# Kernel tuning notes

Hardware: AMD Instinct MI355X
Metric: run time of the kernel (lower is better)

Reference implementation:

```python
import jax, jax.numpy as jnp
import numpy as np

B, C_IN, S = 32, 4, 2048
NF = 256          # CNN filters
H = 256           # LSTM hidden per direction
NH, DH = 8, 64    # heads, single-head size
MH = 512          # multihead size
KSZ, PAD, POOL = 13, 6, 6
SP = (S + 2 * PAD - KSZ + 1) // POOL  # 341: post conv(len-preserving)+maxpool1d length


def _lstm_dir(x, Wih, Whh, b):
    # x: [T, N, C] -- torch LSTM gate order i,f,g,o; b = b_ih + b_hh merged
    N = x.shape[1]
    h0 = jnp.zeros((N, H), x.dtype)
    c0 = jnp.zeros((N, H), x.dtype)

    def step(carry, xt):
        h, c = carry
        g = xt @ Wih.T + h @ Whh.T + b
        i, f, gg, o = jnp.split(g, 4, axis=-1)
        c = jax.nn.sigmoid(f) * c + jax.nn.sigmoid(i) * jnp.tanh(gg)
        h = jax.nn.sigmoid(o) * jnp.tanh(c)
        return (h, c), h

    _, hs = jax.lax.scan(step, (h0, c0), x)
    return hs


def _bilstm(x, Wih, Whh, b):
    fwd = _lstm_dir(x, Wih[0], Whh[0], b[0])
    bwd = _lstm_dir(x[::-1], Wih[1], Whh[1], b[1])[::-1]
    return jnp.concatenate([fwd, bwd], axis=-1)


def _rpe():
    # RelativePosition: |clip(k-q, -(S-1), S-1)| / (S-1); identical across the
    # batch-repeat channels, so compute once then broadcast (same math).
    r = jnp.arange(S)
    d = jnp.abs(jnp.clip(r[None, :] - r[:, None], -(S - 1), S - 1))
    d = d.astype(jnp.float32) / jnp.float32(S - 1)
    # nn.MaxPool2d((9,9), stride=(6,6), padding=1) -> [341, 341]
    return jax.lax.reduce_window(d, -jnp.inf, jax.lax.max, (9, 9), (6, 6), [(1, 1), (1, 1)])


def setup_inputs():
    key = jax.random.key(0)
    ks = jax.random.split(key, 20)
    f = lambda i, shape: jax.random.normal(ks[i], shape, jnp.float32) * 0.05
    return {
        "inputs": jax.random.normal(ks[0], (B, C_IN, S), jnp.float32),
        "conv1_w": f(1, (NF, C_IN, KSZ)),
        "bn1_gamma": jnp.ones((NF,), jnp.float32),
        "bn1_beta": jnp.zeros((NF,), jnp.float32),
        "Wih0": f(2, (2, 4 * H, NF)),
        "Whh0": f(3, (2, 4 * H, H)),
        "b0": f(4, (2, 4 * H)),
        "Wih1": f(5, (2, 4 * H, 2 * H)),
        "Whh1": f(6, (2, 4 * H, H)),
        "b1": f(7, (2, 4 * H)),
        "Qw": f(8, (NH, DH, 2 * H)), "Qb": f(9, (NH, DH)),
        "Kw": f(10, (NH, DH, 2 * H)), "Kb": f(11, (NH, DH)),
        "Vw": f(12, (NH, DH, 2 * H)), "Vb": f(13, (NH, DH)),
        "mh_w": f(14, (MH, NH * DH)), "mh_b": f(15, (MH,)),
    }


def reference(inputs, conv1_w, bn1_gamma, bn1_beta, Wih0, Whh0, b0,
              Wih1, Whh1, b1, Qw, Qb, Kw, Kb, Vw, Vb, mh_w, mh_b):
    # layer1: Conv1d (bias=False, pad=6 keeps length) + BatchNorm1d(eval: mean=0, var=1) + ReLU + MaxPool1d(6)
    x = jax.lax.conv_general_dilated(inputs, conv1_w, (1,), [(PAD, PAD)],
                                     dimension_numbers=('NCH', 'OIH', 'NCH'))
    x = x * (bn1_gamma / jnp.sqrt(1.0 + 1e-5))[None, :, None] + bn1_beta[None, :, None]
    x = jax.nn.relu(x)
    x = jax.lax.reduce_window(x, -jnp.inf, jax.lax.max, (1, 1, POOL), (1, 1, POOL), 'VALID')  # [B,NF,SP]
    x = jnp.transpose(x, (0, 2, 1))  # [B, SP, NF]

    # torch nn.LSTM with batch_first=False fed [B,SP,NF]: scans over axis 0 (batch) -- replicated faithfully.
    x = _bilstm(x, Wih0, Whh0, b0)
    x = _bilstm(x, Wih1, Whh1, b1)  # [B, SP, 2H]
    # (the F_RNN/R_RNN split-and-concat is an identity)

    # per-head Q/K/V (batched over heads), relative attention, dropout off (eval)
    q = jnp.einsum('bsc,hdc->hbsd', x, Qw) + Qb[:, None, None, :]
    k = jnp.einsum('bsc,hdc->hbsd', x, Kw) + Kb[:, None, None, :]
    v = jnp.einsum('bsc,hdc->hbsd', x, Vw) + Vb[:, None, None, :]
    scores = jnp.einsum('hbqd,hbkd->hbqk', q, k) / jnp.sqrt(jnp.float32(DH))
    scores = scores / _rpe()[None, None, :, :]
    p = jax.nn.softmax(scores, axis=-1)
    attn = jax.nn.relu(jnp.einsum('hbqk,hbkd->hbqd', p, v))  # [NH,B,SP,DH]
    cat = jnp.transpose(attn, (1, 2, 0, 3)).reshape(B, SP, NH * DH)
    out = jax.nn.relu(cat @ mh_w.T + mh_b)  # MultiHeadLinear + MHReLU
    return out
```

## Files before the change

kernel.cpp:

```cpp
#include <hip/hip_runtime.h>
#include <math.h>

#define B_    32
#define CIN   4
#define SLEN  2048
#define NF    256
#define HD    256
#define SP    341
#define RTOT  (B_*SP)
#define NH_   8
#define DH_   64
#define GRP   4
#define PSTR  344
#define HS    (SP*HD)

typedef __attribute__((ext_vector_type(8))) short short8;
typedef __attribute__((ext_vector_type(4))) float floatx4;
typedef __attribute__((ext_vector_type(4))) unsigned short ushortx4;

__device__ __forceinline__ float sigmoidf_(float x) { return 1.0f / (1.0f + expf(-x)); }

__device__ __forceinline__ unsigned short f2bf(float x) {
    unsigned int u = __float_as_uint(x);
    unsigned int r = (u + 0x7FFF + ((u >> 16) & 1)) >> 16;
    return (unsigned short)r;
}
__device__ __forceinline__ float bf2f(unsigned short b) {
    return __uint_as_float(((unsigned int)b) << 16);
}

__global__ __launch_bounds__(256)
void conv_pool_k(const float* __restrict__ in, const float* __restrict__ cw,
                 const float* __restrict__ gamma, const float* __restrict__ beta,
                 float* __restrict__ x0)
{
    const int b  = blockIdx.y;
    const int s0 = blockIdx.x * 16;
    const int co = threadIdx.x;
    __shared__ float ins[CIN][16*6 + 12];
    for (int idx = threadIdx.x; idx < CIN*108; idx += 256) {
        int ci = idx / 108, o = idx % 108;
        int pos = 6*s0 - 6 + o;
        ins[ci][o] = (pos >= 0 && pos < SLEN) ? in[(b*CIN + ci)*SLEN + pos] : 0.0f;
    }
    float wreg[52];
    {
        const float4* wp = (const float4*)(cw + co*52);
        #pragma unroll
        for (int j4 = 0; j4 < 13; ++j4) {
            float4 w4 = wp[j4];
            wreg[j4*4+0]=w4.x; wreg[j4*4+1]=w4.y; wreg[j4*4+2]=w4.z; wreg[j4*4+3]=w4.w;
        }
    }
    const float scale = gamma[co] * (1.0f / sqrtf(1.0f + 1e-5f));
    const float shift = beta[co];
    __syncthreads();
    for (int si = 0; si < 16; ++si) {
        int s = s0 + si;
        if (s >= SP) break;
        float win[CIN][18];
        #pragma unroll
        for (int ci = 0; ci < CIN; ++ci)
            #pragma unroll
            for (int o = 0; o < 18; ++o)
                win[ci][o] = ins[ci][6*si + o];
        float m = -1e30f;
        #pragma unroll
        for (int p6 = 0; p6 < 6; ++p6) {
            float acc = 0.0f;
            #pragma unroll
            for (int ci = 0; ci < CIN; ++ci)
                #pragma unroll
                for (int kk = 0; kk < 13; ++kk)
                    acc += win[ci][p6+kk] * wreg[ci*13+kk];
            float val = acc * scale + shift;
            val = fmaxf(val, 0.0f);
            m = fmaxf(m, val);
        }
        x0[(size_t)(b*SP + s)*NF + co] = m;
    }
}

__global__ __launch_bounds__(256)
void pack4_k(const float* __restrict__ W, unsigned short* __restrict__ hi,
             unsigned short* __restrict__ lo, int n4)
{
    int i = blockIdx.x * 256 + threadIdx.x;
    if (i >= n4) return;
    float4 x = *((const float4*)W + i);
    float v[4] = {x.x, x.y, x.z, x.w};
    ushortx4 h, l;
    #pragma unroll
    for (int e = 0; e < 4; ++e) {
        unsigned short hb = f2bf(v[e]);
        h[e] = hb;
        l[e] = f2bf(v[e] - bf2f(hb));
    }
    *((ushortx4*)hi + i) = h;
    *((ushortx4*)lo + i) = l;
}

template<int RELU>
__global__ __launch_bounds__(256)
void gemm_bf_k(const unsigned short* __restrict__ Ahi, const unsigned short* __restrict__ Alo,
               const unsigned short* __restrict__ Bhi, const unsigned short* __restrict__ Blo,
               const float* __restrict__ bias, float* __restrict__ C,
               int M, int N, int K)
{
    const int n0 = blockIdx.x * 128;
    const int m0 = blockIdx.y * 128;
    const int tid = threadIdx.x;
    const int lane = tid & 63;
    const int w = tid >> 6;
    const int wm = w >> 1, wn = w & 1;
    const int ln15 = lane & 15, lq = lane >> 4;

    __shared__ unsigned short AsH[128][40];
    __shared__ unsigned short AsL[128][40];
    __shared__ unsigned short BsH[128][40];
    __shared__ unsigned short BsL[128][40];

    floatx4 acc[4][4];
    #pragma unroll
    for (int i = 0; i < 4; ++i)
        #pragma unroll
        for (int j = 0; j < 4; ++j) acc[i][j] = (floatx4){0.f, 0.f, 0.f, 0.f};

    const int srow = tid >> 2;
    const int scol = (tid & 3) * 8;
    int ra0 = m0 + srow;      if (ra0 >= M) ra0 = M - 1;
    int ra1 = m0 + srow + 64; if (ra1 >= M) ra1 = M - 1;
    const int rb0 = n0 + srow;
    const int rb1 = n0 + srow + 64;

    for (int k0 = 0; k0 < K; k0 += 32) {
        const size_t aoff0 = (size_t)ra0*K + k0 + scol;
        const size_t aoff1 = (size_t)ra1*K + k0 + scol;
        const size_t boff0 = (size_t)rb0*K + k0 + scol;
        const size_t boff1 = (size_t)rb1*K + k0 + scol;
        short8 ah0 = *(const short8*)(Ahi + aoff0);
        short8 ah1 = *(const short8*)(Ahi + aoff1);
        short8 al0 = *(const short8*)(Alo + aoff0);
        short8 al1 = *(const short8*)(Alo + aoff1);
        short8 bh0 = *(const short8*)(Bhi + boff0);
        short8 bh1 = *(const short8*)(Bhi + boff1);
        short8 bl0 = *(const short8*)(Blo + boff0);
        short8 bl1 = *(const short8*)(Blo + boff1);
        *(short8*)&AsH[srow     ][scol] = ah0;
        *(short8*)&AsH[srow + 64][scol] = ah1;
        *(short8*)&AsL[srow     ][scol] = al0;
        *(short8*)&AsL[srow + 64][scol] = al1;
        *(short8*)&BsH[srow     ][scol] = bh0;
        *(short8*)&BsH[srow + 64][scol] = bh1;
        *(short8*)&BsL[srow     ][scol] = bl0;
        *(short8*)&BsL[srow + 64][scol] = bl1;
        __syncthreads();

        short8 fa_h[4], fa_l[4], fb_h[4], fb_l[4];
        #pragma unroll
        for (int mt = 0; mt < 4; ++mt) {
            fa_h[mt] = *(const short8*)&AsH[wm*64 + mt*16 + ln15][lq*8];
            fa_l[mt] = *(const short8*)&AsL[wm*64 + mt*16 + ln15][lq*8];
        }
        #pragma unroll
        for (int nt = 0; nt < 4; ++nt) {
            fb_h[nt] = *(const short8*)&BsH[wn*64 + nt*16 + ln15][lq*8];
            fb_l[nt] = *(const short8*)&BsL[wn*64 + nt*16 + ln15][lq*8];
        }
        #pragma unroll
        for (int mt = 0; mt < 4; ++mt)
            #pragma unroll
            for (int nt = 0; nt < 4; ++nt) {
                acc[mt][nt] = __builtin_amdgcn_mfma_f32_16x16x32_bf16(fa_l[mt], fb_h[nt], acc[mt][nt], 0, 0, 0);
                acc[mt][nt] = __builtin_amdgcn_mfma_f32_16x16x32_bf16(fa_h[mt], fb_l[nt], acc[mt][nt], 0, 0, 0);
                acc[mt][nt] = __builtin_amdgcn_mfma_f32_16x16x32_bf16(fa_h[mt], fb_h[nt], acc[mt][nt], 0, 0, 0);
            }
        __syncthreads();
    }

    #pragma unroll
    for (int nt = 0; nt < 4; ++nt) {
        const int n = n0 + wn*64 + nt*16 + ln15;
        const float bv = bias[n];
        #pragma unroll
        for (int mt = 0; mt < 4; ++mt) {
            const int mbase = m0 + wm*64 + mt*16 + lq*4;
            #pragma unroll
            for (int r = 0; r < 4; ++r) {
                int m = mbase + r;
                if (m < M) {
                    float val = acc[mt][nt][r] + bv;
                    if (RELU) val = fmaxf(val, 0.0f);
                    C[(size_t)m*N + n] = val;
                }
            }
        }
    }
}

__global__ __launch_bounds__(256)
void lstm_step_mfma_k(const float* __restrict__ G,
                      const unsigned short* __restrict__ Whi,
                      const unsigned short* __restrict__ Wlo,
                      const float* __restrict__ h_in,
                      float* __restrict__ h_out,
                      float* __restrict__ c_st,
                      float* __restrict__ x_out,
                      int s)
{
    const int j0 = blockIdx.x * 32;
    const int m0 = blockIdx.y * 32;
    const int d  = blockIdx.z;
    const int t_in = d ? (B_ - 1 - s) : s;
    const int tid = threadIdx.x;
    const int w = tid >> 6, lane = tid & 63;
    const int mhalf = w & 1, gpair = w >> 1;
    const int ln15 = lane & 15, lq = lane >> 4;

    __shared__ float Csh[32][132];

    int am = m0 + mhalf*16 + ln15; if (am > SP-1) am = SP-1;
    const int akoff = lq * 8;
    const float* hA = h_in + (size_t)d*HS + (size_t)am*HD;

    const unsigned short* WhiD = Whi + (size_t)d*1024*256;
    const unsigned short* WloD = Wlo + (size_t)d*1024*256;
    int nrow[4];
    #pragma unroll
    for (int t = 0; t < 4; ++t)
        nrow[t] = (gpair*2 + (t>>1))*256 + j0 + (t&1)*16 + ln15;

    floatx4 acc[4];
    #pragma unroll
    for (int t = 0; t < 4; ++t) acc[t] = (floatx4){0.f, 0.f, 0.f, 0.f};

    #pragma unroll
    for (int kk = 0; kk < 8; ++kk) {
        const int ko = kk*32 + akoff;
        float4 v0 = *(const float4*)(hA + ko);
        float4 v1 = *(const float4*)(hA + ko + 4);
        float vv[8] = {v0.x, v0.y, v0.z, v0.w, v1.x, v1.y, v1.z, v1.w};
        short8 ahi, alo;
        #pragma unroll
        for (int e = 0; e < 8; ++e) {
            unsigned short hb16 = f2bf(vv[e]);
            ahi[e] = (short)hb16;
            alo[e] = (short)f2bf(vv[e] - bf2f(hb16));
        }
        #pragma unroll
        for (int t = 0; t < 4; ++t) {
            short8 bhi = *(const short8*)(WhiD + (size_t)nrow[t]*HD + ko);
            short8 blo = *(const short8*)(WloD + (size_t)nrow[t]*HD + ko);
            acc[t] = __builtin_amdgcn_mfma_f32_16x16x32_bf16(alo, bhi, acc[t], 0, 0, 0);
            acc[t] = __builtin_amdgcn_mfma_f32_16x16x32_bf16(ahi, blo, acc[t], 0, 0, 0);
            acc[t] = __builtin_amdgcn_mfma_f32_16x16x32_bf16(ahi, bhi, acc[t], 0, 0, 0);
        }
    }

    #pragma unroll
    for (int t = 0; t < 4; ++t) {
        int col = gpair*64 + (t>>1)*32 + (t&1)*16 + ln15;
        int rb  = mhalf*16 + lq*4;
        #pragma unroll
        for (int r = 0; r < 4; ++r)
            Csh[rb + r][col] = acc[t][r];
    }
    __syncthreads();

    const int emloc = tid >> 3;
    const int ej4   = (tid & 7) * 4;
    const int em    = m0 + emloc;
    if (em < SP) {
        size_t gb = ((size_t)t_in*SP + em)*2048 + (size_t)d*1024 + j0 + ej4;
        float4 gi4 = *(const float4*)&G[gb];
        float4 gf4 = *(const float4*)&G[gb + 256];
        float4 gg4 = *(const float4*)&G[gb + 512];
        float4 go4 = *(const float4*)&G[gb + 768];
        size_t cbase = ((size_t)d*SP + em)*HD + j0 + ej4;
        float4 cold = *(float4*)&c_st[cbase];
        float hv[4];
        #pragma unroll
        for (int e = 0; e < 4; ++e) {
            float gi = Csh[emloc][     ej4+e] + (&gi4.x)[e];
            float gf = Csh[emloc][32 + ej4+e] + (&gf4.x)[e];
            float gg = Csh[emloc][64 + ej4+e] + (&gg4.x)[e];
            float go = Csh[emloc][96 + ej4+e] + (&go4.x)[e];
            float cn = sigmoidf_(gf)*(&cold.x)[e] + sigmoidf_(gi)*tanhf(gg);
            (&cold.x)[e] = cn;
            hv[e] = sigmoidf_(go)*tanhf(cn);
        }
        *(float4*)&c_st[cbase] = cold;
        float4 ho; ho.x = hv[0]; ho.y = hv[1]; ho.z = hv[2]; ho.w = hv[3];
        *(float4*)&h_out[cbase] = ho;
        *(float4*)&x_out[((size_t)t_in*SP + em)*512 + d*HD + j0 + ej4] = ho;
    }
}

__global__ __launch_bounds__(256)
void scores_k(const float* __restrict__ q, const float* __restrict__ k,
              float* __restrict__ P, int g)
{
    const int h = blockIdx.z, bl = blockIdx.y, bg = g*GRP + bl;
    const int q0 = (blockIdx.x / 6) * 64;
    const int k0 = (blockIdx.x % 6) * 64;
    const int tid = threadIdx.x;
    __shared__ float qs[64][68];
    __shared__ float ks[64][68];
    {
        int jr = tid >> 2, c16 = (tid & 3) * 16;
        int qq = q0 + jr; if (qq > SP-1) qq = SP-1;
        int kr = k0 + jr; if (kr > SP-1) kr = SP-1;
        const float* qp = &q[((size_t)bg*SP + qq)*512 + h*64 + c16];
        const float* kp = &k[((size_t)bg*SP + kr)*512 + h*64 + c16];
        #pragma unroll
        for (int u = 0; u < 4; ++u) {
            *(float4*)&qs[jr][c16 + u*4] = *(const float4*)(qp + u*4);
            *(float4*)&ks[jr][c16 + u*4] = *(const float4*)(kp + u*4);
        }
    }
    __syncthreads();
    const int tx = tid & 15, ty = tid >> 4;
    float acc[4][4];
    #pragma unroll
    for (int i = 0; i < 4; ++i)
        #pragma unroll
        for (int j = 0; j < 4; ++j) acc[i][j] = 0.0f;
    for (int d4 = 0; d4 < 64; d4 += 4) {
        float4 a[4], b[4];
        #pragma unroll
        for (int i = 0; i < 4; ++i) a[i] = *(const float4*)&qs[ty + 16*i][d4];
        #pragma unroll
        for (int j = 0; j < 4; ++j) b[j] = *(const float4*)&ks[tx + 16*j][d4];
        #pragma unroll
        for (int i = 0; i < 4; ++i)
            #pragma unroll
            for (int j = 0; j < 4; ++j)
                acc[i][j] += a[i].x*b[j].x + a[i].y*b[j].y + a[i].z*b[j].z + a[i].w*b[j].w;
    }
    #pragma unroll
    for (int i = 0; i < 4; ++i) {
        int qq = q0 + ty + 16*i;
        if (qq >= SP) continue;
        int r0 = 6*qq - 1; if (r0 < 0) r0 = 0;
        int r1 = 6*qq + 7; if (r1 > SLEN-1) r1 = SLEN-1;
        size_t rowb = ((size_t)(h*GRP + bl)*SP + qq) * PSTR;
        #pragma unroll
        for (int j = 0; j < 4; ++j) {
            int kk = k0 + tx + 16*j;
            if (kk >= SP) continue;
            int c0 = 6*kk - 1; if (c0 < 0) c0 = 0;
            int c1 = 6*kk + 7;
            int dd1 = c1 - r0; if (dd1 < 0) dd1 = -dd1;
            int dd2 = r1 - c0; if (dd2 < 0) dd2 = -dd2;
            int den = dd1 > dd2 ? dd1 : dd2;
            P[rowb + kk] = (acc[i][j] * 0.125f) * 2047.0f / (float)den;
        }
    }
}

__global__ __launch_bounds__(256)
void softmax_k(float* __restrict__ P)
{
    const int tid = threadIdx.x;
    const int row = blockIdx.x * 4 + (tid >> 6);
    const int lane = tid & 63;
    float* rp = P + (size_t)row * PSTR;
    float v[6];
    float m = -1e30f;
    #pragma unroll
    for (int i = 0; i < 6; ++i) {
        int col = lane + 64*i;
        v[i] = (col < SP) ? rp[col] : -1e30f;
        m = fmaxf(m, v[i]);
    }
    #pragma unroll
    for (int o = 1; o < 64; o <<= 1) m = fmaxf(m, __shfl_xor(m, o, 64));
    float s = 0.0f;
    #pragma unroll
    for (int i = 0; i < 6; ++i) {
        v[i] = expf(v[i] - m);
        s += v[i];
    }
    #pragma unroll
    for (int o = 1; o < 64; o <<= 1) s += __shfl_xor(s, o, 64);
    float inv = 1.0f / s;
    #pragma unroll
    for (int i = 0; i < 6; ++i) {
        int col = lane + 64*i;
        if (col < SP) rp[col] = v[i] * inv;
    }
}

__global__ __launch_bounds__(256)
void pv_k(const float* __restrict__ P, const float* __restrict__ v,
          float* __restrict__ cat, int g)
{
    const int h = blockIdx.z, bl = blockIdx.y, bg = g*GRP + bl;
    const int q0 = blockIdx.x * 64;
    const int tid = threadIdx.x;
    __shared__ float ps[64][68];
    __shared__ float vs[64][68];
    const int tx = tid & 15, ty = tid >> 4;
    float acc[4][4];
    #pragma unroll
    for (int i = 0; i < 4; ++i)
        #pragma unroll
        for (int j = 0; j < 4; ++j) acc[i][j] = 0.0f;

    for (int kc = 0; kc < 6; ++kc) {
        const int kk0 = kc * 64;
        {
            int jr = tid >> 2, c16 = (tid & 3) * 16;
            int qq = q0 + jr; if (qq > SP-1) qq = SP-1;
            const float* pp = P + ((size_t)(h*GRP + bl)*SP + qq)*PSTR + kk0 + c16;
            #pragma unroll
            for (int u = 0; u < 4; ++u) {
                float4 w = *(const float4*)(pp + u*4);
                int klb = c16 + u*4;
                float vals[4] = {w.x, w.y, w.z, w.w};
                #pragma unroll
                for (int e = 0; e < 4; ++e)
                    ps[klb + e][jr] = (kk0 + klb + e < SP) ? vals[e] : 0.0f;
            }
        }
        {
            int jr = tid >> 2, c16 = (tid & 3) * 16;
            int kr = kk0 + jr; if (kr > SP-1) kr = SP-1;
            const float* vp = &v[((size_t)bg*SP + kr)*512 + h*64 + c16];
            #pragma unroll
            for (int u = 0; u < 4; ++u)
                *(float4*)&vs[jr][c16 + u*4] = *(const float4*)(vp + u*4);
        }
        __syncthreads();
        for (int kk = 0; kk < 64; ++kk) {
            float4 a4 = *(const float4*)&ps[kk][ty*4];
            float4 b4 = *(const float4*)&vs[kk][tx*4];
            float av[4] = {a4.x, a4.y, a4.z, a4.w};
            float bv[4] = {b4.x, b4.y, b4.z, b4.w};
            #pragma unroll
            for (int i = 0; i < 4; ++i)
                #pragma unroll
                for (int j = 0; j < 4; ++j)
                    acc[i][j] += av[i] * bv[j];
        }
        __syncthreads();
    }
    #pragma unroll
    for (int i = 0; i < 4; ++i) {
        int qq = q0 + ty*4 + i;
        if (qq >= SP) continue;
        float4 r;
        r.x = fmaxf(acc[i][0], 0.0f);
        r.y = fmaxf(acc[i][1], 0.0f);
        r.z = fmaxf(acc[i][2], 0.0f);
        r.w = fmaxf(acc[i][3], 0.0f);
        *(float4*)&cat[((size_t)bg*SP + qq)*512 + h*64 + tx*4] = r;
    }
}

extern "C" void kernel_launch(void* const* d_in, const int* in_sizes, int n_in,
                              void* d_out, int out_size, void* d_ws, size_t ws_size,
                              hipStream_t stream)
{
    (void)in_sizes; (void)n_in; (void)out_size; (void)ws_size;
    const float* in    = (const float*)d_in[0];
    const float* cw    = (const float*)d_in[1];
    const float* gamma = (const float*)d_in[2];
    const float* beta  = (const float*)d_in[3];
    const float* Wih0  = (const float*)d_in[4];
    const float* Whh0  = (const float*)d_in[5];
    const float* b0    = (const float*)d_in[6];
    const float* Wih1  = (const float*)d_in[7];
    const float* Whh1  = (const float*)d_in[8];
    const float* b1    = (const float*)d_in[9];
    const float* Qw    = (const float*)d_in[10];
    const float* Qb    = (const float*)d_in[11];
    const float* Kw    = (const float*)d_in[12];
    const float* Kb    = (const float*)d_in[13];
    const float* Vw    = (const float*)d_in[14];
    const float* Vb    = (const float*)d_in[15];
    const float* mhw   = (const float*)d_in[16];
    const float* mhb   = (const float*)d_in[17];
    float* out = (float*)d_out;

    float* x0 = (float*)d_ws;
    float* G  = x0 + (size_t)RTOT*NF;
    float* x1 = G  + (size_t)RTOT*2048;
    float* x2 = x1 + (size_t)RTOT*512;
    float* hb = x2 + (size_t)RTOT*512;
    float* cb = hb + (size_t)2*2*SP*HD;

    float* qbuf = G;
    float* kbuf = G + (size_t)RTOT*512;
    float* vbuf = G + (size_t)2*RTOT*512;
    float* P    = G + (size_t)3*RTOT*512;
    float* cat  = x1;
    const size_t hsz = (size_t)2*SP*HD;

    unsigned short* wih0_hi = (unsigned short*)x2;
    unsigned short* wih0_lo = wih0_hi + (size_t)524288;
    unsigned short* x0_hi   = wih0_lo + (size_t)524288;
    unsigned short* x0_lo   = x0_hi   + (size_t)2793472;
    unsigned short* whh0_hi = (unsigned short*)x0;
    unsigned short* whh0_lo = whh0_hi + (size_t)524288;
    unsigned short* whh1_hi = whh0_lo + (size_t)524288;
    unsigned short* whh1_lo = whh1_hi + (size_t)524288;
    unsigned short* wih1_hi = whh1_lo + (size_t)524288;
    unsigned short* wih1_lo = wih1_hi + (size_t)1048576;
    unsigned short* x1_hi = (unsigned short*)x2;
    unsigned short* x1_lo = x1_hi + (size_t)5586944;
    unsigned short* x2_hi = (unsigned short*)x1;
    unsigned short* x2_lo = x2_hi + (size_t)5586944;
    float* gslack = P + (size_t)NH_*GRP*SP*PSTR;
    unsigned short* qw_hi = (unsigned short*)gslack;
    unsigned short* qw_lo = qw_hi + (size_t)262144;
    unsigned short* kw_hi = qw_lo + (size_t)262144;
    unsigned short* kw_lo = kw_hi + (size_t)262144;
    unsigned short* vw_hi = kw_lo + (size_t)262144;
    unsigned short* vw_lo = vw_hi + (size_t)262144;
    unsigned short* mw_hi = vw_lo + (size_t)262144;
    unsigned short* mw_lo = mw_hi + (size_t)262144;
    unsigned short* cat_hi = (unsigned short*)x2;
    unsigned short* cat_lo = cat_hi + (size_t)5586944;

    #define PACKGRID(n4) dim3(((n4) + 255) / 256)

    conv_pool_k<<<dim3(22, B_), 256, 0, stream>>>(in, cw, gamma, beta, x0);
    pack4_k<<<PACKGRID(131072), 256, 0, stream>>>(Wih0, wih0_hi, wih0_lo, 131072);
    pack4_k<<<PACKGRID(698368), 256, 0, stream>>>(x0, x0_hi, x0_lo, 698368);
    gemm_bf_k<0><<<dim3(16, 86), 256, 0, stream>>>(x0_hi, x0_lo, wih0_hi, wih0_lo, b0, G, RTOT, 2048, 256);
    pack4_k<<<PACKGRID(131072), 256, 0, stream>>>(Whh0, whh0_hi, whh0_lo, 131072);
    pack4_k<<<PACKGRID(131072), 256, 0, stream>>>(Whh1, whh1_hi, whh1_lo, 131072);
    pack4_k<<<PACKGRID(262144), 256, 0, stream>>>(Wih1, wih1_hi, wih1_lo, 262144);
    hipMemsetAsync(hb, 0, 2*hsz*sizeof(float), stream);
    hipMemsetAsync(cb, 0, hsz*sizeof(float), stream);
    for (int s = 0; s < B_; ++s) {
        float* hin  = hb + (size_t)(s & 1) * hsz;
        float* hout = hb + (size_t)((s+1) & 1) * hsz;
        lstm_step_mfma_k<<<dim3(8, 11, 2), 256, 0, stream>>>(
            G, whh0_hi, whh0_lo, hin, hout, cb, x1, s);
    }
    pack4_k<<<PACKGRID(1396736), 256, 0, stream>>>(x1, x1_hi, x1_lo, 1396736);
    gemm_bf_k<0><<<dim3(16, 86), 256, 0, stream>>>(x1_hi, x1_lo, wih1_hi, wih1_lo, b1, G, RTOT, 2048, 512);
    hipMemsetAsync(hb, 0, 2*hsz*sizeof(float), stream);
    hipMemsetAsync(cb, 0, hsz*sizeof(float), stream);
    for (int s = 0; s < B_; ++s) {
        float* hin  = hb + (size_t)(s & 1) * hsz;
        float* hout = hb + (size_t)((s+1) & 1) * hsz;
        lstm_step_mfma_k<<<dim3(8, 11, 2), 256, 0, stream>>>(
            G, whh1_hi, whh1_lo, hin, hout, cb, x2, s);
    }
    pack4_k<<<PACKGRID(1396736), 256, 0, stream>>>(x2, x2_hi, x2_lo, 1396736);
    pack4_k<<<PACKGRID(65536), 256, 0, stream>>>(Qw,  qw_hi, qw_lo, 65536);
    pack4_k<<<PACKGRID(65536), 256, 0, stream>>>(Kw,  kw_hi, kw_lo, 65536);
    pack4_k<<<PACKGRID(65536), 256, 0, stream>>>(Vw,  vw_hi, vw_lo, 65536);
    pack4_k<<<PACKGRID(65536), 256, 0, stream>>>(mhw, mw_hi, mw_lo, 65536);
    gemm_bf_k<0><<<dim3(4, 86), 256, 0, stream>>>(x2_hi, x2_lo, qw_hi, qw_lo, Qb, qbuf, RTOT, 512, 512);
    gemm_bf_k<0><<<dim3(4, 86), 256, 0, stream>>>(x2_hi, x2_lo, kw_hi, kw_lo, Kb, kbuf, RTOT, 512, 512);
    gemm_bf_k<0><<<dim3(4, 86), 256, 0, stream>>>(x2_hi, x2_lo, vw_hi, vw_lo, Vb, vbuf, RTOT, 512, 512);
    for (int g = 0; g < B_/GRP; ++g) {
        scores_k <<<dim3(36, GRP, NH_), 256, 0, stream>>>(qbuf, kbuf, P, g);
        softmax_k<<<dim3(NH_*GRP*SP/4), 256, 0, stream>>>(P);
        pv_k     <<<dim3(6, GRP, NH_), 256, 0, stream>>>(P, vbuf, cat, g);
    }
    pack4_k<<<PACKGRID(1396736), 256, 0, stream>>>(cat, cat_hi, cat_lo, 1396736);
    gemm_bf_k<1><<<dim3(4, 86), 256, 0, stream>>>(cat_hi, cat_lo, mw_hi, mw_lo, mhb, out, RTOT, 512, 512);
    #undef PACKGRID
}
```

Measured before the change: 1.758 ms.

## Fuse bf16 hi/lo split into producers and interleave packed GEMM operand layout

Producers (conv, LSTM step, PV) now write activations directly as interleaved bf16 hi/lo pairs. This removes the separate pack4 passes over large fp32 activation buffers. The GEMM reads one interleaved operand per matrix, stages it into XOR-swizzled shared memory, and puts the barrier before the LDS write instead of at the end of the k-loop. The changes save global traffic and launches, at the cost of more scattered 2-byte stores in the producers and reworked buffer aliasing.

```diff
diff --git a/kernel.cpp b/kernel.cpp
--- a/kernel.cpp
+++ b/kernel.cpp
@@ -17,6 +17,7 @@
 typedef __attribute__((ext_vector_type(8))) short short8;
 typedef __attribute__((ext_vector_type(4))) float floatx4;
 typedef __attribute__((ext_vector_type(4))) unsigned short ushortx4;
+typedef __attribute__((ext_vector_type(8))) unsigned short ushort8;
 
 __device__ __forceinline__ float sigmoidf_(float x) { return 1.0f / (1.0f + expf(-x)); }
 
@@ -29,10 +30,11 @@
     return __uint_as_float(((unsigned int)b) << 16);
 }
 
+
 __global__ __launch_bounds__(256)
 void conv_pool_k(const float* __restrict__ in, const float* __restrict__ cw,
                  const float* __restrict__ gamma, const float* __restrict__ beta,
-                 float* __restrict__ x0)
+                 unsigned short* __restrict__ x0p)
 {
     const int b  = blockIdx.y;
     const int s0 = blockIdx.x * 16;
@@ -77,7 +79,11 @@
             val = fmaxf(val, 0.0f);
             m = fmaxf(m, val);
         }
-        x0[(size_t)(b*SP + s)*NF + co] = m;
+        unsigned short hb_ = f2bf(m);
+        unsigned short lb_ = f2bf(m - bf2f(hb_));
+        size_t rb = (size_t)(b*SP + s)*512 + (size_t)(co >> 3)*16 + (co & 7);
+        x0p[rb]     = hb_;
+        x0p[rb + 8] = lb_;
     }
 }
 
@@ -100,10 +106,28 @@
     *((ushortx4*)lo + i) = l;
 }
 
+__global__ __launch_bounds__(256)
+void pack8_k(const float* __restrict__ W, unsigned short* __restrict__ O, int n8)
+{
+    int i = blockIdx.x * 256 + threadIdx.x;
+    if (i >= n8) return;
+    const float4* wp = (const float4*)W + (size_t)i*2;
+    float4 a = wp[0], b = wp[1];
+    float v[8] = {a.x,a.y,a.z,a.w,b.x,b.y,b.z,b.w};
+    ushort8 h, l;
+    #pragma unroll
+    for (int e = 0; e < 8; ++e) {
+        unsigned short hb = f2bf(v[e]);
+        h[e] = hb;
+        l[e] = f2bf(v[e] - bf2f(hb));
+    }
+    *(ushort8*)(O + (size_t)i*16)     = h;
+    *(ushort8*)(O + (size_t)i*16 + 8) = l;
+}
+
 template<int RELU>
 __global__ __launch_bounds__(256)
-void gemm_bf_k(const unsigned short* __restrict__ Ahi, const unsigned short* __restrict__ Alo,
-               const unsigned short* __restrict__ Bhi, const unsigned short* __restrict__ Blo,
+void gemm_bf_k(const unsigned short* __restrict__ Ap, const unsigned short* __restrict__ Bp,
                const float* __restrict__ bias, float* __restrict__ C,
                int M, int N, int K)
 {
@@ -114,11 +138,11 @@
     const int w = tid >> 6;
     const int wm = w >> 1, wn = w & 1;
     const int ln15 = lane & 15, lq = lane >> 4;
-
-    __shared__ unsigned short AsH[128][40];
-    __shared__ unsigned short AsL[128][40];
-    __shared__ unsigned short BsH[128][40];
-    __shared__ unsigned short BsL[128][40];
+    const int l8 = lane >> 3, lj = lane & 7;
+    const size_t rstr = 2*(size_t)K;
+
+    __shared__ unsigned short As[128*64];
+    __shared__ unsigned short Bs[128*64];
 
     floatx4 acc[4][4];
     #pragma unroll
@@ -126,46 +150,39 @@
         #pragma unroll
         for (int j = 0; j < 4; ++j) acc[i][j] = (floatx4){0.f, 0.f, 0.f, 0.f};
 
-    const int srow = tid >> 2;
-    const int scol = (tid & 3) * 8;
-    int ra0 = m0 + srow;      if (ra0 >= M) ra0 = M - 1;
-    int ra1 = m0 + srow + 64; if (ra1 >= M) ra1 = M - 1;
-    const int rb0 = n0 + srow;
-    const int rb1 = n0 + srow + 64;
+    int rloc[4];
+    #pragma unroll
+    for (int c = 0; c < 4; ++c) rloc[c] = w*32 + c*8 + l8;
+    const int spos = lj ^ (l8 & 7);
 
     for (int k0 = 0; k0 < K; k0 += 32) {
-        const size_t aoff0 = (size_t)ra0*K + k0 + scol;
-        const size_t aoff1 = (size_t)ra1*K + k0 + scol;
-        const size_t boff0 = (size_t)rb0*K + k0 + scol;
-        const size_t boff1 = (size_t)rb1*K + k0 + scol;
-        short8 ah0 = *(const short8*)(Ahi + aoff0);
-        short8 ah1 = *(const short8*)(Ahi + aoff1);
-        short8 al0 = *(const short8*)(Alo + aoff0);
-        short8 al1 = *(const short8*)(Alo + aoff1);
-        short8 bh0 = *(const short8*)(Bhi + boff0);
-        short8 bh1 = *(const short8*)(Bhi + boff1);
-        short8 bl0 = *(const short8*)(Blo + boff0);
-        short8 bl1 = *(const short8*)(Blo + boff1);
-        *(short8*)&AsH[srow     ][scol] = ah0;
-        *(short8*)&AsH[srow + 64][scol] = ah1;
-        *(short8*)&AsL[srow     ][scol] = al0;
-        *(short8*)&AsL[srow + 64][scol] = al1;
-        *(short8*)&BsH[srow     ][scol] = bh0;
-        *(short8*)&BsH[srow + 64][scol] = bh1;
-        *(short8*)&BsL[srow     ][scol] = bl0;
-        *(short8*)&BsL[srow + 64][scol] = bl1;
+        short8 va[4], vb[4];
+        #pragma unroll
+        for (int c = 0; c < 4; ++c) {
+            int gra = m0 + rloc[c]; if (gra >= M) gra = M - 1;
+            va[c] = *(const short8*)(Ap + (size_t)gra*rstr + k0*2 + lj*8);
+            vb[c] = *(const short8*)(Bp + (size_t)(n0 + rloc[c])*rstr + k0*2 + lj*8);
+        }
         __syncthreads();
+        #pragma unroll
+        for (int c = 0; c < 4; ++c) {
+            *(short8*)&As[rloc[c]*64 + spos*8] = va[c];
+            *(short8*)&Bs[rloc[c]*64 + spos*8] = vb[c];
+        }
+        __syncthreads();
 
         short8 fa_h[4], fa_l[4], fb_h[4], fb_l[4];
         #pragma unroll
         for (int mt = 0; mt < 4; ++mt) {
-            fa_h[mt] = *(const short8*)&AsH[wm*64 + mt*16 + ln15][lq*8];
-            fa_l[mt] = *(const short8*)&AsL[wm*64 + mt*16 + ln15][lq*8];
+            const int lr = wm*64 + mt*16 + ln15;
+            fa_h[mt] = *(const short8*)&As[lr*64 + (((lq*2  ) ^ (lr&7))*8)];
+            fa_l[mt] = *(const short8*)&As[lr*64 + (((lq*2+1) ^ (lr&7))*8)];
         }
         #pragma unroll
         for (int nt = 0; nt < 4; ++nt) {
-            fb_h[nt] = *(const short8*)&BsH[wn*64 + nt*16 + ln15][lq*8];
-            fb_l[nt] = *(const short8*)&BsL[wn*64 + nt*16 + ln15][lq*8];
+            const int lr = wn*64 + nt*16 + ln15;
+            fb_h[nt] = *(const short8*)&Bs[lr*64 + (((lq*2  ) ^ (lr&7))*8)];
+            fb_l[nt] = *(const short8*)&Bs[lr*64 + (((lq*2+1) ^ (lr&7))*8)];
         }
         #pragma unroll
         for (int mt = 0; mt < 4; ++mt)
@@ -175,7 +192,6 @@
                 acc[mt][nt] = __builtin_amdgcn_mfma_f32_16x16x32_bf16(fa_h[mt], fb_l[nt], acc[mt][nt], 0, 0, 0);
                 acc[mt][nt] = __builtin_amdgcn_mfma_f32_16x16x32_bf16(fa_h[mt], fb_h[nt], acc[mt][nt], 0, 0, 0);
             }
-        __syncthreads();
     }
 
     #pragma unroll
@@ -205,7 +221,7 @@
                       const float* __restrict__ h_in,
                       float* __restrict__ h_out,
                       float* __restrict__ c_st,
-                      float* __restrict__ x_out,
+                      unsigned short* __restrict__ x_out,
                       int s)
 {
     const int j0 = blockIdx.x * 32;
@@ -292,7 +308,17 @@
         *(float4*)&c_st[cbase] = cold;
         float4 ho; ho.x = hv[0]; ho.y = hv[1]; ho.z = hv[2]; ho.w = hv[3];
         *(float4*)&h_out[cbase] = ho;
-        *(float4*)&x_out[((size_t)t_in*SP + em)*512 + d*HD + j0 + ej4] = ho;
+        const int colg = d*HD + j0 + ej4;
+        size_t xb = ((size_t)t_in*SP + em)*1024 + (size_t)(colg >> 3)*16 + (colg & 7);
+        ushortx4 xh, xl;
+        #pragma unroll
+        for (int e = 0; e < 4; ++e) {
+            unsigned short hb16 = f2bf(hv[e]);
+            xh[e] = hb16;
+            xl[e] = f2bf(hv[e] - bf2f(hb16));
+        }
+        *(ushortx4*)&x_out[xb]     = xh;
+        *(ushortx4*)&x_out[xb + 8] = xl;
     }
 }
 
@@ -393,7 +419,7 @@
 
 __global__ __launch_bounds__(256)
 void pv_k(const float* __restrict__ P, const float* __restrict__ v,
-          float* __restrict__ cat, int g)
+          unsigned short* __restrict__ catp, int g)
 {
     const int h = blockIdx.z, bl = blockIdx.y, bg = g*GRP + bl;
     const int q0 = blockIdx.x * 64;
@@ -449,12 +475,22 @@
     for (int i = 0; i < 4; ++i) {
         int qq = q0 + ty*4 + i;
         if (qq >= SP) continue;
-        float4 r;
-        r.x = fmaxf(acc[i][0], 0.0f);
-        r.y = fmaxf(acc[i][1], 0.0f);
-        r.z = fmaxf(acc[i][2], 0.0f);
-        r.w = fmaxf(acc[i][3], 0.0f);
-        *(float4*)&cat[((size_t)bg*SP + qq)*512 + h*64 + tx*4] = r;
+        float r[4];
+        r[0] = fmaxf(acc[i][0], 0.0f);
+        r[1] = fmaxf(acc[i][1], 0.0f);
+        r[2] = fmaxf(acc[i][2], 0.0f);
+        r[3] = fmaxf(acc[i][3], 0.0f);
+        const int colg = h*64 + tx*4;
+        size_t xb = ((size_t)bg*SP + qq)*1024 + (size_t)(colg >> 3)*16 + (colg & 7);
+        ushortx4 xh, xl;
+        #pragma unroll
+        for (int e = 0; e < 4; ++e) {
+            unsigned short hb16 = f2bf(r[e]);
+            xh[e] = hb16;
+            xl[e] = f2bf(r[e] - bf2f(hb16));
+        }
+        *(ushortx4*)&catp[xb]     = xh;
+        *(ushortx4*)&catp[xb + 8] = xl;
     }
 }
 
@@ -494,76 +530,61 @@
     float* kbuf = G + (size_t)RTOT*512;
     float* vbuf = G + (size_t)2*RTOT*512;
     float* P    = G + (size_t)3*RTOT*512;
-    float* cat  = x1;
     const size_t hsz = (size_t)2*SP*HD;
 
-    unsigned short* wih0_hi = (unsigned short*)x2;
-    unsigned short* wih0_lo = wih0_hi + (size_t)524288;
-    unsigned short* x0_hi   = wih0_lo + (size_t)524288;
-    unsigned short* x0_lo   = x0_hi   + (size_t)2793472;
-    unsigned short* whh0_hi = (unsigned short*)x0;
+    unsigned short* x0p = (unsigned short*)x0;
+    unsigned short* whh1_hi = (unsigned short*)x0;
+    unsigned short* whh1_lo = whh1_hi + (size_t)524288;
+    unsigned short* wih0_p  = (unsigned short*)x2;
+    unsigned short* wih1_p  = wih0_p + (size_t)1048576;
+    unsigned short* whh0_hi = wih1_p + (size_t)2097152;
     unsigned short* whh0_lo = whh0_hi + (size_t)524288;
-    unsigned short* whh1_hi = whh0_lo + (size_t)524288;
-    unsigned short* whh1_lo = whh1_hi + (size_t)524288;
-    unsigned short* wih1_hi = whh1_lo + (size_t)524288;
-    unsigned short* wih1_lo = wih1_hi + (size_t)1048576;
-    unsigned short* x1_hi = (unsigned short*)x2;
-    unsigned short* x1_lo = x1_hi + (size_t)5586944;
-    unsigned short* x2_hi = (unsigned short*)x1;
-    unsigned short* x2_lo = x2_hi + (size_t)5586944;
+    unsigned short* x1p  = (unsigned short*)x1;
+    unsigned short* catp = (unsigned short*)x1;
+    unsigned short* x2p = (unsigned short*)x2;
     float* gslack = P + (size_t)NH_*GRP*SP*PSTR;
-    unsigned short* qw_hi = (unsigned short*)gslack;
-    unsigned short* qw_lo = qw_hi + (size_t)262144;
-    unsigned short* kw_hi = qw_lo + (size_t)262144;
-    unsigned short* kw_lo = kw_hi + (size_t)262144;
-    unsigned short* vw_hi = kw_lo + (size_t)262144;
-    unsigned short* vw_lo = vw_hi + (size_t)262144;
-    unsigned short* mw_hi = vw_lo + (size_t)262144;
-    unsigned short* mw_lo = mw_hi + (size_t)262144;
-    unsigned short* cat_hi = (unsigned short*)x2;
-    unsigned short* cat_lo = cat_hi + (size_t)5586944;
-
-    #define PACKGRID(n4) dim3(((n4) + 255) / 256)
-
-    conv_pool_k<<<dim3(22, B_), 256, 0, stream>>>(in, cw, gamma, beta, x0);
-    pack4_k<<<PACKGRID(131072), 256, 0, stream>>>(Wih0, wih0_hi, wih0_lo, 131072);
-    pack4_k<<<PACKGRID(698368), 256, 0, stream>>>(x0, x0_hi, x0_lo, 698368);
-    gemm_bf_k<0><<<dim3(16, 86), 256, 0, stream>>>(x0_hi, x0_lo, wih0_hi, wih0_lo, b0, G, RTOT, 2048, 256);
+    unsigned short* qw_p = (unsigned short*)gslack;
+    unsigned short* kw_p = qw_p + (size_t)524288;
+    unsigned short* vw_p = kw_p + (size_t)524288;
+    unsigned short* mw_p = vw_p + (size_t)524288;
+
+    #define PACKGRID(n) dim3(((n) + 255) / 256)
+
+    conv_pool_k<<<dim3(22, B_), 256, 0, stream>>>(in, cw, gamma, beta, x0p);
+    pack8_k<<<PACKGRID(65536), 256, 0, stream>>>(Wih0, wih0_p, 65536);
+    gemm_bf_k<0><<<dim3(16, 86), 256, 0, stream>>>(x0p, wih0_p, b0, G, RTOT, 2048, 256);
     pack4_k<<<PACKGRID(131072), 256, 0, stream>>>(Whh0, whh0_hi, whh0_lo, 131072);
     pack4_k<<<PACKGRID(131072), 256, 0, stream>>>(Whh1, whh1_hi, whh1_lo, 131072);
-    pack4_k<<<PACKGRID(262144), 256, 0, stream>>>(Wih1, wih1_hi, wih1_lo, 262144);
+    pack8_k<<<PACKGRID(131072), 256, 0, stream>>>(Wih1, wih1_p, 131072);
     hipMemsetAsync(hb, 0, 2*hsz*sizeof(float), stream);
     hipMemsetAsync(cb, 0, hsz*sizeof(float), stream);
     for (int s = 0; s < B_; ++s) {
         float* hin  = hb + (size_t)(s & 1) * hsz;
         float* hout = hb + (size_t)((s+1) & 1) * hsz;
         lstm_step_mfma_k<<<dim3(8, 11, 2), 256, 0, stream>>>(
-            G, whh0_hi, whh0_lo, hin, hout, cb, x1, s);
-    }
-    pack4_k<<<PACKGRID(1396736), 256, 0, stream>>>(x1, x1_hi, x1_lo, 1396736);
-    gemm_bf_k<0><<<dim3(16, 86), 256, 0, stream>>>(x1_hi, x1_lo, wih1_hi, wih1_lo, b1, G, RTOT, 2048, 512);
+            G, whh0_hi, whh0_lo, hin, hout, cb, x1p, s);
+    }
+    gemm_bf_k<0><<<dim3(16, 86), 256, 0, stream>>>(x1p, wih1_p, b1, G, RTOT, 2048, 512);
     hipMemsetAsync(hb, 0, 2*hsz*sizeof(float), stream);
     hipMemsetAsync(cb, 0, hsz*sizeof(float), stream);
     for (int s = 0; s < B_; ++s) {
         float* hin  = hb + (size_t)(s & 1) * hsz;
         float* hout = hb + (size_t)((s+1) & 1) * hsz;
         lstm_step_mfma_k<<<dim3(8, 11, 2), 256, 0, stream>>>(
-            G, whh1_hi, whh1_lo, hin, hout, cb, x2, s);
-    }
-    pack4_k<<<PACKGRID(1396736), 256, 0, stream>>>(x2, x2_hi, x2_lo, 1396736);
-    pack4_k<<<PACKGRID(65536), 256, 0, stream>>>(Qw,  qw_hi, qw_lo, 65536);
-    pack4_k<<<PACKGRID(65536), 256, 0, stream>>>(Kw,  kw_hi, kw_lo, 65536);
-    pack4_k<<<PACKGRID(65536), 256, 0, stream>>>(Vw,  vw_hi, vw_lo, 65536);
-    pack4_k<<<PACKGRID(65536), 256, 0, stream>>>(mhw, mw_hi, mw_lo, 65536);
-    gemm_bf_k<0><<<dim3(4, 86), 256, 0, stream>>>(x2_hi, x2_lo, qw_hi, qw_lo, Qb, qbuf, RTOT, 512, 512);
-    gemm_bf_k<0><<<dim3(4, 86), 256, 0, stream>>>(x2_hi, x2_lo, kw_hi, kw_lo, Kb, kbuf, RTOT, 512, 512);
-    gemm_bf_k<0><<<dim3(4, 86), 256, 0, stream>>>(x2_hi, x2_lo, vw_hi, vw_lo, Vb, vbuf, RTOT, 512, 512);
+            G, whh1_hi, whh1_lo, hin, hout, cb, x2p, s);
+    }
+    pack8_k<<<PACKGRID(32768), 256, 0, stream>>>(Qw,  qw_p, 32768);
+    pack8_k<<<PACKGRID(32768), 256, 0, stream>>>(Kw,  kw_p, 32768);
+    pack8_k<<<PACKGRID(32768), 256, 0, stream>>>(Vw,  vw_p, 32768);
+    pack8_k<<<PACKGRID(32768), 256, 0, stream>>>(mhw, mw_p, 32768);
+    gemm_bf_k<0><<<dim3(4, 86), 256, 0, stream>>>(x2p, qw_p, Qb, qbuf, RTOT, 512, 512);
+    gemm_bf_k<0><<<dim3(4, 86), 256, 0, stream>>>(x2p, kw_p, Kb, kbuf, RTOT, 512, 512);
+    gemm_bf_k<0><<<dim3(4, 86), 256, 0, stream>>>(x2p, vw_p, Vb, vbuf, RTOT, 512, 512);
     for (int g = 0; g < B_/GRP; ++g) {
         scores_k <<<dim3(36, GRP, NH_), 256, 0, stream>>>(qbuf, kbuf, P, g);
         softmax_k<<<dim3(NH_*GRP*SP/4), 256, 0, stream>>>(P);
-        pv_k     <<<dim3(6, GRP, NH_), 256, 0, stream>>>(P, vbuf, cat, g);
-    }
-    pack4_k<<<PACKGRID(1396736), 256, 0, stream>>>(cat, cat_hi, cat_lo, 1396736);
-    gemm_bf_k<1><<<dim3(4, 86), 256, 0, stream>>>(cat_hi, cat_lo, mw_hi, mw_lo, mhb, out, RTOT, 512, 512);
+        pv_k     <<<dim3(6, GRP, NH_), 256, 0, stream>>>(P, vbuf, catp, g);
+    }
+    gemm_bf_k<1><<<dim3(4, 86), 256, 0, stream>>>(catp, mw_p, mhb, out, RTOT, 512, 512);
     #undef PACKGRID
 }
```

New measurement: 1.693 ms. -3.7%, faster.
